# Performance work log

Measured on AMD Instinct MI355X. Metric: run time of the kernel, lower is better.

## Reference

```python
import jax, jax.numpy as jnp
import numpy as np

BATCH = 1024
DIM = 1024      # input_size == hidden_size (required by h0 = z.repeat(...))
BAR = 32
EPS = 1e-5


def setup_inputs() -> dict:
    key = jax.random.key(0)
    ks = jax.random.split(key, 13)
    s_in = 1.0 / np.sqrt(DIM)
    return {
        "z": jax.random.normal(ks[0], (BATCH, DIM), dtype=jnp.float32),
        "bn_gamma": jnp.ones((DIM,), jnp.float32),
        "bn_beta": jnp.zeros((DIM,), jnp.float32),
        # PyTorch LSTM params, gate order (i, f, g, o), shape (4H, in)
        "W_ih0": jax.random.uniform(ks[1], (4 * DIM, DIM), jnp.float32, -s_in, s_in),
        "W_hh0": jax.random.uniform(ks[2], (4 * DIM, DIM), jnp.float32, -s_in, s_in),
        "b_ih0": jax.random.uniform(ks[3], (4 * DIM,), jnp.float32, -s_in, s_in),
        "b_hh0": jax.random.uniform(ks[4], (4 * DIM,), jnp.float32, -s_in, s_in),
        "W_ih1": jax.random.uniform(ks[5], (4 * DIM, DIM), jnp.float32, -s_in, s_in),
        "W_hh1": jax.random.uniform(ks[6], (4 * DIM, DIM), jnp.float32, -s_in, s_in),
        "b_ih1": jax.random.uniform(ks[7], (4 * DIM,), jnp.float32, -s_in, s_in),
        "b_hh1": jax.random.uniform(ks[8], (4 * DIM,), jnp.float32, -s_in, s_in),
        "W_lin": jax.random.uniform(ks[9], (DIM, DIM), jnp.float32, -s_in, s_in),
        "b_lin": jax.random.uniform(ks[10], (DIM,), jnp.float32, -s_in, s_in),
    }


def _lstm_cell(x_proj, h, c, W_hh, b_hh):
    # x_proj already contains x @ W_ih^T + b_ih
    gates = x_proj + h @ W_hh.T + b_hh          # (B, 4H)
    i, f, g, o = jnp.split(gates, 4, axis=-1)   # PyTorch gate order i,f,g,o
    c_new = jax.nn.sigmoid(f) * c + jax.nn.sigmoid(i) * jnp.tanh(g)
    h_new = jax.nn.sigmoid(o) * jnp.tanh(c_new)
    return h_new, c_new


def reference(z, bn_gamma, bn_beta, W_ih0, W_hh0, b_ih0, b_hh0,
              W_ih1, W_hh1, b_ih1, b_hh1, W_lin, b_lin):
    # BatchNorm1d in training mode (batch statistics, biased variance)
    mean = jnp.mean(z, axis=0)
    var = jnp.var(z, axis=0)
    zn = (z - mean) * jax.lax.rsqrt(var + EPS) * bn_gamma + bn_beta  # (B, D)

    # h0 = c0 = zn for both layers (init_hidden repeats z num_hidden times)
    # Layer-0 input is the constant zn every step -> precompute its projection
    x0_proj = zn @ W_ih0.T + b_ih0  # (B, 4H)

    def step(carry, _):
        h0, c0, h1, c1 = carry
        h0, c0 = _lstm_cell(x0_proj, h0, c0, W_hh0, b_hh0)
        x1_proj = h0 @ W_ih1.T + b_ih1
        h1, c1 = _lstm_cell(x1_proj, h1, c1, W_hh1, b_hh1)
        return (h0, c0, h1, c1), h1

    _, feats = jax.lax.scan(step, (zn, zn, zn, zn), None, length=BAR)
    feat = jnp.transpose(feats, (1, 0, 2))      # (B, bar, H)
    return feat @ W_lin.T + b_lin
```

## Files before the change

kernel.cpp:

```cpp
#include <hip/hip_runtime.h>

#define DEV __device__ __forceinline__

typedef unsigned short u16;
using bf16x8 = __attribute__((ext_vector_type(8))) __bf16;
using f32x4  = __attribute__((ext_vector_type(4))) float;

DEV u16 f2bf(float f){
  unsigned u = __float_as_uint(f);
  u += 0x7fffu + ((u >> 16) & 1u);
  return (u16)(u >> 16);
}
DEV float sigf(float x){ return 1.f / (1.f + __expf(-x)); }
DEV float tanh_(float x){ return 2.f / (1.f + __expf(-2.f*x)) - 1.f; }

DEV void async16(const u16* g, u16* l){
  __builtin_amdgcn_global_load_lds(
      (const __attribute__((address_space(1))) unsigned int*)g,
      (__attribute__((address_space(3))) unsigned int*)l, 16, 0, 0);
}

__global__ void bn_stats(const float* __restrict__ z, float* __restrict__ ps, float* __restrict__ pq){
  int bx = blockIdx.x; int rg = bx >> 2, cg = bx & 3;
  int c = cg*256 + threadIdx.x;
  float s = 0.f, q = 0.f;
  for (int r = rg*64; r < rg*64 + 64; ++r){ float v = z[r*1024 + c]; s += v; q += v*v; }
  ps[rg*1024 + c] = s; pq[rg*1024 + c] = q;
}

__global__ void bn_fin(const float* __restrict__ ps, const float* __restrict__ pq,
                       const float* __restrict__ gam, const float* __restrict__ bet,
                       float* __restrict__ sc, float* __restrict__ sh){
  int c = blockIdx.x*256 + threadIdx.x;
  float s = 0.f, q = 0.f;
  for (int rg = 0; rg < 16; ++rg){ s += ps[rg*1024 + c]; q += pq[rg*1024 + c]; }
  float mean = s * (1.f/1024.f);
  float var  = q * (1.f/1024.f) - mean*mean;
  float k = gam[c] * rsqrtf(var + 1e-5f);
  sc[c] = k; sh[c] = bet[c] - mean*k;
}

__global__ void bn_norm(const float* __restrict__ z, const float* __restrict__ sc, const float* __restrict__ sh,
                        u16* __restrict__ h0, u16* __restrict__ h1,
                        float* __restrict__ c0, float* __restrict__ c1){
  int bx = blockIdx.x; int rg = bx >> 2, cg = bx & 3;
  int c = cg*256 + threadIdx.x;
  float k = sc[c], b = sh[c];
  for (int r = rg*64; r < rg*64 + 64; ++r){
    float v = z[r*1024 + c]*k + b;
    u16 hv = f2bf(v);
    h0[r*1024 + c] = hv; h1[r*1024 + c] = hv;
    c0[r*1024 + c] = v;  c1[r*1024 + c] = v;
  }
}

__global__ void pack_w(const float* __restrict__ src0, const float* __restrict__ src1,
                       int KloA, int K, int permute, u16* __restrict__ dst){
  int c = blockIdx.x*4 + (threadIdx.x >> 6);
  int lane = threadIdx.x & 63;
  int j = c & 3, wn = (c>>2)&1, ksub = (c>>3)&1;
  int rest = c >> 4;
  int nkt = K >> 6;
  int kt = rest % nkt, bx = rest / nkt;
  int rn = bx*128 + wn*64 + j*16 + (lane & 15);
  int row = rn;
  if (permute){ int gate=(rn>>4)&3; int u=(rn&15)|((rn>>6)<<4); row=(gate<<10)+u; }
  int k0 = kt*64 + ksub*32 + (lane>>4)*8;
  const float* s; int kk;
  if (k0 < KloA){ s = src0; kk = k0; } else { s = src1; kk = k0 - KloA; }
  const float4* v = (const float4*)(s + (size_t)row*1024 + kk);
  float4 a = v[0], b = v[1];
  ushort4 o0; o0.x=f2bf(a.x); o0.y=f2bf(a.y); o0.z=f2bf(a.z); o0.w=f2bf(a.w);
  ushort4 o1; o1.x=f2bf(b.x); o1.y=f2bf(b.y); o1.z=f2bf(b.z); o1.w=f2bf(b.w);
  ushort4* d = (ushort4*)(dst + ((size_t)c<<9) + lane*8);
  d[0]=o0; d[1]=o1;
}

__global__ void bias_k(const float* __restrict__ bi0, const float* __restrict__ bh0,
                       const float* __restrict__ bi1, const float* __restrict__ bh1,
                       float* __restrict__ bx0, float* __restrict__ b1){
  int c = blockIdx.x*256 + threadIdx.x;
  int gate = (c>>4)&3; int u = (c&15) | ((c>>6)<<4); int r = (gate<<10) + u;
  bx0[c] = bi0[r] + bh0[r];
  b1[c]  = bi1[r] + bh1[r];
}

template<int MODE>
DEV void gemm_core(int bx, int by,
                   const u16* __restrict__ A0, const u16* __restrict__ A1, int KloA,
                   const u16* __restrict__ Bp, int K,
                   const float* __restrict__ add, float* __restrict__ cst,
                   u16* __restrict__ hout, u16* __restrict__ hout2,
                   float* __restrict__ outf,
                   u16* sA)
{
  const int t = threadIdx.x;
  const int lane = t & 63;
  const int w = t >> 6, wm = w >> 1, wn = w & 1;
  const int m0 = by*128, n0 = bx*128;

  f32x4 acc[4][4];
#pragma unroll
  for (int i = 0; i < 4; ++i)
#pragma unroll
    for (int j = 0; j < 4; ++j) acc[i][j] = (f32x4){0.f,0.f,0.f,0.f};

  const int srow = t >> 3;
  const int kswz = (((t & 7) ^ ((t >> 3) & 7)) << 3);
  const int nkt = K >> 6;

  auto stageA = [&](int kt, int b){
    const int k0 = kt << 6;
    const u16* aPart; int kk;
    if (k0 < KloA){ aPart = A0; kk = k0; } else { aPart = A1; kk = k0 - KloA; }
    u16* dst = sA + b*8192;
#pragma unroll
    for (int p = 0; p < 4; ++p)
      async16(aPart + (size_t)(m0 + p*32 + srow)*1024 + kk + kswz,
              dst + p*2048 + t*8);
  };

  const u16* BpL = Bp + lane*8;
  auto loadB = [&](bf16x8* b, int kt, int ksub){
    const u16* p = BpL + (((((size_t)bx*nkt + kt)*2 + ksub)*2 + wn) << 11);
#pragma unroll
    for (int j = 0; j < 4; ++j) b[j] = *(const bf16x8*)(p + (size_t)j*512);
  };

  const int rsel = lane >> 4;
  const int rxor = lane & 7;

  bf16x8 bP[4], bQ[4];
  stageA(0, 0); stageA(1, 1);
  loadB(bP, 0, 0);
  asm volatile("s_waitcnt vmcnt(0)" ::: "memory");
  __builtin_amdgcn_sched_barrier(0);
  __builtin_amdgcn_s_barrier();
  __builtin_amdgcn_sched_barrier(0);

  for (int kt = 0; kt < nkt; ++kt){
    const u16* pA = sA + (kt % 3)*8192;
    loadB(bQ, kt, 1);
    {
      bf16x8 af[4];
#pragma unroll
      for (int i = 0; i < 4; ++i){
        int ra = wm*64 + i*16 + (lane & 15);
        int sl = ((0*4 + rsel) ^ rxor) << 3;
        af[i] = *(const bf16x8*)&pA[ra*64 + sl];
      }
      __builtin_amdgcn_s_setprio(1);
#pragma unroll
      for (int i = 0; i < 4; ++i)
#pragma unroll
        for (int j = 0; j < 4; ++j)
          acc[i][j] = __builtin_amdgcn_mfma_f32_16x16x32_bf16(af[i], bP[j], acc[i][j], 0, 0, 0);
      __builtin_amdgcn_s_setprio(0);
    }
    {
      int ktn = (kt + 1 < nkt) ? kt + 1 : nkt - 1;
      int kts = (kt + 2 < nkt) ? kt + 2 : nkt - 1;
      loadB(bP, ktn, 0);
      stageA(kts, (kt + 2) % 3);
      bf16x8 af[4];
#pragma unroll
      for (int i = 0; i < 4; ++i){
        int ra = wm*64 + i*16 + (lane & 15);
        int sl = ((1*4 + rsel) ^ rxor) << 3;
        af[i] = *(const bf16x8*)&pA[ra*64 + sl];
      }
      __builtin_amdgcn_s_setprio(1);
#pragma unroll
      for (int i = 0; i < 4; ++i)
#pragma unroll
        for (int j = 0; j < 4; ++j)
          acc[i][j] = __builtin_amdgcn_mfma_f32_16x16x32_bf16(af[i], bQ[j], acc[i][j], 0, 0, 0);
      __builtin_amdgcn_s_setprio(0);
    }
    asm volatile("s_waitcnt vmcnt(8)" ::: "memory");
    __builtin_amdgcn_sched_barrier(0);
    __builtin_amdgcn_s_barrier();
    __builtin_amdgcn_sched_barrier(0);
  }

  const int s  = lane & 15;
  const int rq = (lane >> 4) * 4;

  if constexpr (MODE == 0 || MODE == 3){
    const int ldc = (MODE == 0) ? 4096 : 1024;
#pragma unroll
    for (int j = 0; j < 4; ++j){
      int col = n0 + wn*64 + j*16 + s;
      float bj = add[col];
#pragma unroll
      for (int i = 0; i < 4; ++i){
        int rowb = m0 + wm*64 + i*16 + rq;
#pragma unroll
        for (int r = 0; r < 4; ++r)
          outf[(size_t)(rowb + r)*ldc + col] = acc[i][j][r] + bj;
      }
    }
  } else {
    const int u = s + ((bx*2 + wn) << 4);
    int cidx[4]; float bj[4];
#pragma unroll
    for (int j = 0; j < 4; ++j){
      cidx[j] = n0 + wn*64 + j*16 + s;
      if (MODE == 2) bj[j] = add[cidx[j]];
    }
#pragma unroll
    for (int i = 0; i < 4; ++i){
      int rowb = m0 + wm*64 + i*16 + rq;
#pragma unroll
      for (int r = 0; r < 4; ++r){
        int row = rowb + r;
        float g0, g1, g2, g3;
        if (MODE == 1){
          const float* xp = add + (size_t)row*4096;
          g0 = acc[i][0][r] + xp[cidx[0]];
          g1 = acc[i][1][r] + xp[cidx[1]];
          g2 = acc[i][2][r] + xp[cidx[2]];
          g3 = acc[i][3][r] + xp[cidx[3]];
        } else {
          g0 = acc[i][0][r] + bj[0];
          g1 = acc[i][1][r] + bj[1];
          g2 = acc[i][2][r] + bj[2];
          g3 = acc[i][3][r] + bj[3];
        }
        float ig = sigf(g0), fg = sigf(g1), gg = tanh_(g2), og = sigf(g3);
        size_t si = (size_t)row*1024 + u;
        float cn = fg * cst[si] + ig * gg;
        cst[si] = cn;
        float hn = og * tanh_(cn);
        u16 hb = f2bf(hn);
        hout[si] = hb;
        if (MODE == 2) hout2[(size_t)row*32768 + u] = hb;
      }
    }
  }
}

template<int MODE, int SWZ>
__global__ __launch_bounds__(256)
void gemm_k(const u16* __restrict__ A0, const u16* __restrict__ Bp, int K,
            const float* __restrict__ add, float* __restrict__ outf)
{
  __shared__ __align__(16) u16 sA[3*8192];
  int bx = blockIdx.x, by = blockIdx.y;
  if constexpr (SWZ){
    int lin = by * (int)gridDim.x + bx;
    int xcd = lin & 7, idx = lin >> 3;
    by = xcd*32 + (idx >> 3);
    bx = idx & 7;
  }
  gemm_core<MODE>(bx, by, A0, nullptr, 1<<20, Bp, K, add,
                  nullptr, nullptr, nullptr, outf, sA);
}

__global__ __launch_bounds__(256)
void fused_step(const u16* __restrict__ h0in, const u16* __restrict__ h1in,
                const u16* __restrict__ Whh0p, const u16* __restrict__ W1p,
                const float* __restrict__ X0p, const float* __restrict__ B1,
                float* __restrict__ C0, float* __restrict__ C1,
                u16* __restrict__ h0out, u16* __restrict__ h1out,
                u16* __restrict__ feats, int roles)
{
  __shared__ __align__(16) u16 sA[3*8192];
  int by = blockIdx.y, isL0;
  if (roles == 0){ isL0 = (by >= 8); by &= 7; }
  else isL0 = (roles == 1);
  if (isL0)
    gemm_core<1>(blockIdx.x, by, h0in, nullptr, 1<<20, Whh0p, 1024, X0p,
                 C0, h0out, nullptr, nullptr, sA);
  else
    gemm_core<2>(blockIdx.x, by, h0in, h1in, 1024, W1p, 2048, B1,
                 C1, h1out, feats, nullptr, sA);
}

extern "C" void kernel_launch(void* const* d_in, const int* in_sizes, int n_in,
                              void* d_out, int out_size, void* d_ws, size_t ws_size,
                              hipStream_t stream)
{
  (void)in_sizes; (void)n_in; (void)out_size; (void)ws_size;
  const float* z    = (const float*)d_in[0];
  const float* gam  = (const float*)d_in[1];
  const float* bet  = (const float*)d_in[2];
  const float* Wih0 = (const float*)d_in[3];
  const float* Whh0 = (const float*)d_in[4];
  const float* bih0 = (const float*)d_in[5];
  const float* bhh0 = (const float*)d_in[6];
  const float* Wih1 = (const float*)d_in[7];
  const float* Whh1 = (const float*)d_in[8];
  const float* bih1 = (const float*)d_in[9];
  const float* bhh1 = (const float*)d_in[10];
  const float* Wlin = (const float*)d_in[11];
  const float* blin = (const float*)d_in[12];
  float* out = (float*)d_out;

  char* p = (char*)d_ws;
  auto alloc = [&](size_t b) -> void* { void* r = (void*)p; p += (b + 255) & ~(size_t)255; return r; };
  u16*  Wih0p = (u16*)alloc((size_t)4096*1024*2);
  u16*  Whh0p = (u16*)alloc((size_t)4096*1024*2);
  u16*  W1p   = (u16*)alloc((size_t)4096*2048*2);
  u16*  Wlinp = (u16*)alloc((size_t)1024*1024*2);
  float* Bx0  = (float*)alloc(4096*4);
  float* B1   = (float*)alloc(4096*4);
  float* X0p  = (float*)alloc((size_t)1024*4096*4);
  u16*  H0a   = (u16*)alloc((size_t)1024*1024*2);
  u16*  H0b   = (u16*)alloc((size_t)1024*1024*2);
  u16*  H1a   = (u16*)alloc((size_t)1024*1024*2);
  u16*  H1b   = (u16*)alloc((size_t)1024*1024*2);
  float* C0   = (float*)alloc((size_t)1024*1024*4);
  float* C1   = (float*)alloc((size_t)1024*1024*4);
  u16*  Feats = (u16*)alloc((size_t)1024*32*1024*2);
  float* PS   = (float*)alloc(16*1024*4);
  float* PQ   = (float*)alloc(16*1024*4);
  float* Sc   = (float*)alloc(1024*4);
  float* Sh   = (float*)alloc(1024*4);

  bn_stats<<<64, 256, 0, stream>>>(z, PS, PQ);
  bn_fin<<<4, 256, 0, stream>>>(PS, PQ, gam, bet, Sc, Sh);
  bn_norm<<<64, 256, 0, stream>>>(z, Sc, Sh, H0a, H1a, C0, C1);
  pack_w<<<2048, 256, 0, stream>>>(Wih0, Wih0, 1<<20, 1024, 1, Wih0p);
  pack_w<<<2048, 256, 0, stream>>>(Whh0, Whh0, 1<<20, 1024, 1, Whh0p);
  pack_w<<<4096, 256, 0, stream>>>(Wih1, Whh1, 1024, 2048, 1, W1p);
  pack_w<<< 512, 256, 0, stream>>>(Wlin, Wlin, 1<<20, 1024, 0, Wlinp);
  bias_k<<<16, 256, 0, stream>>>(bih0, bhh0, bih1, bhh1, Bx0, B1);

  gemm_k<0,0><<<dim3(32,8), 256, 0, stream>>>(H0a, Wih0p, 1024, Bx0, X0p);

  u16* h0b[2] = {H0a, H0b};
  u16* h1b[2] = {H1a, H1b};

  fused_step<<<dim3(32,8), 256, 0, stream>>>(h0b[0], nullptr, Whh0p, W1p, X0p, B1,
                                             C0, C1, h0b[1], nullptr, nullptr, 1);
  for (int t = 0; t < 31; ++t){
    fused_step<<<dim3(32,16), 256, 0, stream>>>(
        h0b[(t+1)&1], h1b[t&1], Whh0p, W1p, X0p, B1,
        C0, C1, h0b[t&1], h1b[(t+1)&1], Feats + (size_t)t*1024, 0);
  }
  fused_step<<<dim3(32,8), 256, 0, stream>>>(h0b[0], h1b[1], Whh0p, W1p, X0p, B1,
                                             C0, C1, nullptr, h1b[0], Feats + (size_t)31*1024, 2);

  gemm_k<3,1><<<dim3(8,256), 256, 0, stream>>>(Feats, Wlinp, 1024, blin, out);
}
```

Measured before the change: 1.482 ms.

## Enlarge GEMM block tile to 256x128 with 8 waves and double-buffered LDS

Changes the GEMM tile from 128x128 with 4 waves to 256x128 with 8 waves. Each wave now owns 32 rows by all 128 columns, so every wave loads the full B slice, and the packed weight layout is changed to match. The A staging moves from a triple buffer to a double buffer, the grids are halved, and launch bounds are set to 512 threads with 2 blocks per SM. The intent is more A reuse per weight fetch and fewer blocks per step, at the cost of more registers per wave, a shallower prefetch pipeline and fewer blocks in flight (256 per fused step instead of 512).

```diff
diff --git a/kernel.cpp b/kernel.cpp
--- a/kernel.cpp
+++ b/kernel.cpp
@@ -58,17 +58,17 @@
                        int KloA, int K, int permute, u16* __restrict__ dst){
   int c = blockIdx.x*4 + (threadIdx.x >> 6);
   int lane = threadIdx.x & 63;
-  int j = c & 3, wn = (c>>2)&1, ksub = (c>>3)&1;
+  int j = c & 7, ksub = (c>>3)&1;
   int rest = c >> 4;
   int nkt = K >> 6;
   int kt = rest % nkt, bx = rest / nkt;
-  int rn = bx*128 + wn*64 + j*16 + (lane & 15);
+  int rn = bx*128 + j*16 + (lane & 15);
   int row = rn;
   if (permute){ int gate=(rn>>4)&3; int u=(rn&15)|((rn>>6)<<4); row=(gate<<10)+u; }
   int k0 = kt*64 + ksub*32 + (lane>>4)*8;
-  const float* s; int kk;
-  if (k0 < KloA){ s = src0; kk = k0; } else { s = src1; kk = k0 - KloA; }
-  const float4* v = (const float4*)(s + (size_t)row*1024 + kk);
+  const float* sp; int kk;
+  if (k0 < KloA){ sp = src0; kk = k0; } else { sp = src1; kk = k0 - KloA; }
+  const float4* v = (const float4*)(sp + (size_t)row*1024 + kk);
   float4 a = v[0], b = v[1];
   ushort4 o0; o0.x=f2bf(a.x); o0.y=f2bf(a.y); o0.z=f2bf(a.z); o0.w=f2bf(a.w);
   ushort4 o1; o1.x=f2bf(b.x); o1.y=f2bf(b.y); o1.z=f2bf(b.z); o1.w=f2bf(b.w);
@@ -96,16 +96,15 @@
 {
   const int t = threadIdx.x;
   const int lane = t & 63;
-  const int w = t >> 6, wm = w >> 1, wn = w & 1;
-  const int m0 = by*128, n0 = bx*128;
-
-  f32x4 acc[4][4];
-#pragma unroll
-  for (int i = 0; i < 4; ++i)
-#pragma unroll
-    for (int j = 0; j < 4; ++j) acc[i][j] = (f32x4){0.f,0.f,0.f,0.f};
-
-  const int srow = t >> 3;
+  const int wm = t >> 6;
+  const int m0 = by*256, n0 = bx*128;
+
+  f32x4 acc[2][8];
+#pragma unroll
+  for (int i = 0; i < 2; ++i)
+#pragma unroll
+    for (int j = 0; j < 8; ++j) acc[i][j] = (f32x4){0.f,0.f,0.f,0.f};
+
   const int kswz = (((t & 7) ^ ((t >> 3) & 7)) << 3);
   const int nkt = K >> 6;
 
@@ -113,25 +112,25 @@
     const int k0 = kt << 6;
     const u16* aPart; int kk;
     if (k0 < KloA){ aPart = A0; kk = k0; } else { aPart = A1; kk = k0 - KloA; }
-    u16* dst = sA + b*8192;
+    u16* dst = sA + b*16384;
 #pragma unroll
     for (int p = 0; p < 4; ++p)
-      async16(aPart + (size_t)(m0 + p*32 + srow)*1024 + kk + kswz,
-              dst + p*2048 + t*8);
+      async16(aPart + (size_t)(m0 + p*64 + (t>>3))*1024 + kk + kswz,
+              dst + p*4096 + t*8);
   };
 
   const u16* BpL = Bp + lane*8;
   auto loadB = [&](bf16x8* b, int kt, int ksub){
-    const u16* p = BpL + (((((size_t)bx*nkt + kt)*2 + ksub)*2 + wn) << 11);
-#pragma unroll
-    for (int j = 0; j < 4; ++j) b[j] = *(const bf16x8*)(p + (size_t)j*512);
+    const u16* p = BpL + ((((size_t)bx*nkt + kt)*2 + ksub) << 12);
+#pragma unroll
+    for (int j = 0; j < 8; ++j) b[j] = *(const bf16x8*)(p + (size_t)j*512);
   };
 
   const int rsel = lane >> 4;
   const int rxor = lane & 7;
 
-  bf16x8 bP[4], bQ[4];
-  stageA(0, 0); stageA(1, 1);
+  bf16x8 bP[8], bQ[8];
+  stageA(0, 0);
   loadB(bP, 0, 0);
   asm volatile("s_waitcnt vmcnt(0)" ::: "memory");
   __builtin_amdgcn_sched_barrier(0);
@@ -139,41 +138,41 @@
   __builtin_amdgcn_sched_barrier(0);
 
   for (int kt = 0; kt < nkt; ++kt){
-    const u16* pA = sA + (kt % 3)*8192;
+    const u16* pA = sA + (kt & 1)*16384;
     loadB(bQ, kt, 1);
+    { int kts = (kt + 1 < nkt) ? kt + 1 : nkt - 1;
+      stageA(kts, (kt + 1) & 1); }
     {
-      bf16x8 af[4];
-#pragma unroll
-      for (int i = 0; i < 4; ++i){
-        int ra = wm*64 + i*16 + (lane & 15);
+      bf16x8 af[2];
+#pragma unroll
+      for (int i = 0; i < 2; ++i){
+        int ra = wm*32 + i*16 + (lane & 15);
         int sl = ((0*4 + rsel) ^ rxor) << 3;
         af[i] = *(const bf16x8*)&pA[ra*64 + sl];
       }
       __builtin_amdgcn_s_setprio(1);
 #pragma unroll
-      for (int i = 0; i < 4; ++i)
-#pragma unroll
-        for (int j = 0; j < 4; ++j)
+      for (int i = 0; i < 2; ++i)
+#pragma unroll
+        for (int j = 0; j < 8; ++j)
           acc[i][j] = __builtin_amdgcn_mfma_f32_16x16x32_bf16(af[i], bP[j], acc[i][j], 0, 0, 0);
       __builtin_amdgcn_s_setprio(0);
     }
+    { int ktn = (kt + 1 < nkt) ? kt + 1 : nkt - 1;
+      loadB(bP, ktn, 0); }
     {
-      int ktn = (kt + 1 < nkt) ? kt + 1 : nkt - 1;
-      int kts = (kt + 2 < nkt) ? kt + 2 : nkt - 1;
-      loadB(bP, ktn, 0);
-      stageA(kts, (kt + 2) % 3);
-      bf16x8 af[4];
-#pragma unroll
-      for (int i = 0; i < 4; ++i){
-        int ra = wm*64 + i*16 + (lane & 15);
+      bf16x8 af[2];
+#pragma unroll
+      for (int i = 0; i < 2; ++i){
+        int ra = wm*32 + i*16 + (lane & 15);
         int sl = ((1*4 + rsel) ^ rxor) << 3;
         af[i] = *(const bf16x8*)&pA[ra*64 + sl];
       }
       __builtin_amdgcn_s_setprio(1);
 #pragma unroll
-      for (int i = 0; i < 4; ++i)
-#pragma unroll
-        for (int j = 0; j < 4; ++j)
+      for (int i = 0; i < 2; ++i)
+#pragma unroll
+        for (int j = 0; j < 8; ++j)
           acc[i][j] = __builtin_amdgcn_mfma_f32_16x16x32_bf16(af[i], bQ[j], acc[i][j], 0, 0, 0);
       __builtin_amdgcn_s_setprio(0);
     }
@@ -189,75 +188,78 @@
   if constexpr (MODE == 0 || MODE == 3){
     const int ldc = (MODE == 0) ? 4096 : 1024;
 #pragma unroll
-    for (int j = 0; j < 4; ++j){
-      int col = n0 + wn*64 + j*16 + s;
+    for (int j = 0; j < 8; ++j){
+      int col = n0 + j*16 + s;
       float bj = add[col];
 #pragma unroll
-      for (int i = 0; i < 4; ++i){
-        int rowb = m0 + wm*64 + i*16 + rq;
+      for (int i = 0; i < 2; ++i){
+        int rowb = m0 + wm*32 + i*16 + rq;
 #pragma unroll
         for (int r = 0; r < 4; ++r)
           outf[(size_t)(rowb + r)*ldc + col] = acc[i][j][r] + bj;
       }
     }
   } else {
-    const int u = s + ((bx*2 + wn) << 4);
-    int cidx[4]; float bj[4];
-#pragma unroll
-    for (int j = 0; j < 4; ++j){
-      cidx[j] = n0 + wn*64 + j*16 + s;
-      if (MODE == 2) bj[j] = add[cidx[j]];
-    }
-#pragma unroll
-    for (int i = 0; i < 4; ++i){
-      int rowb = m0 + wm*64 + i*16 + rq;
+    float bj[8];
+    if constexpr (MODE == 2){
+#pragma unroll
+      for (int j = 0; j < 8; ++j) bj[j] = add[n0 + j*16 + s];
+    }
+#pragma unroll
+    for (int i = 0; i < 2; ++i){
+      int rowb = m0 + wm*32 + i*16 + rq;
 #pragma unroll
       for (int r = 0; r < 4; ++r){
         int row = rowb + r;
-        float g0, g1, g2, g3;
-        if (MODE == 1){
-          const float* xp = add + (size_t)row*4096;
-          g0 = acc[i][0][r] + xp[cidx[0]];
-          g1 = acc[i][1][r] + xp[cidx[1]];
-          g2 = acc[i][2][r] + xp[cidx[2]];
-          g3 = acc[i][3][r] + xp[cidx[3]];
-        } else {
-          g0 = acc[i][0][r] + bj[0];
-          g1 = acc[i][1][r] + bj[1];
-          g2 = acc[i][2][r] + bj[2];
-          g3 = acc[i][3][r] + bj[3];
+#pragma unroll
+        for (int half = 0; half < 2; ++half){
+          float g0, g1, g2, g3;
+          if (MODE == 1){
+            const float* xp = add + (size_t)row*4096 + n0;
+            g0 = acc[i][half*4+0][r] + xp[(half*4+0)*16 + s];
+            g1 = acc[i][half*4+1][r] + xp[(half*4+1)*16 + s];
+            g2 = acc[i][half*4+2][r] + xp[(half*4+2)*16 + s];
+            g3 = acc[i][half*4+3][r] + xp[(half*4+3)*16 + s];
+          } else {
+            g0 = acc[i][half*4+0][r] + bj[half*4+0];
+            g1 = acc[i][half*4+1][r] + bj[half*4+1];
+            g2 = acc[i][half*4+2][r] + bj[half*4+2];
+            g3 = acc[i][half*4+3][r] + bj[half*4+3];
+          }
+          float ig = sigf(g0), fg = sigf(g1), gg = tanh_(g2), og = sigf(g3);
+          int u = s + ((bx*2 + half) << 4);
+          size_t si = (size_t)row*1024 + u;
+          float cn = fg * cst[si] + ig * gg;
+          cst[si] = cn;
+          float hn = og * tanh_(cn);
+          u16 hb = f2bf(hn);
+          hout[si] = hb;
+          if (MODE == 2) hout2[(size_t)row*32768 + u] = hb;
         }
-        float ig = sigf(g0), fg = sigf(g1), gg = tanh_(g2), og = sigf(g3);
-        size_t si = (size_t)row*1024 + u;
-        float cn = fg * cst[si] + ig * gg;
-        cst[si] = cn;
-        float hn = og * tanh_(cn);
-        u16 hb = f2bf(hn);
-        hout[si] = hb;
-        if (MODE == 2) hout2[(size_t)row*32768 + u] = hb;
       }
     }
   }
 }
 
 template<int MODE, int SWZ>
-__global__ __launch_bounds__(256)
+__global__ __launch_bounds__(512, 2)
 void gemm_k(const u16* __restrict__ A0, const u16* __restrict__ Bp, int K,
             const float* __restrict__ add, float* __restrict__ outf)
 {
-  __shared__ __align__(16) u16 sA[3*8192];
+  __shared__ __align__(16) u16 sA[2*16384];
   int bx = blockIdx.x, by = blockIdx.y;
   if constexpr (SWZ){
     int lin = by * (int)gridDim.x + bx;
     int xcd = lin & 7, idx = lin >> 3;
-    by = xcd*32 + (idx >> 3);
+    int ypt = (int)gridDim.y >> 3;
+    by = xcd*ypt + (idx >> 3);
     bx = idx & 7;
   }
   gemm_core<MODE>(bx, by, A0, nullptr, 1<<20, Bp, K, add,
                   nullptr, nullptr, nullptr, outf, sA);
 }
 
-__global__ __launch_bounds__(256)
+__global__ __launch_bounds__(512, 2)
 void fused_step(const u16* __restrict__ h0in, const u16* __restrict__ h1in,
                 const u16* __restrict__ Whh0p, const u16* __restrict__ W1p,
                 const float* __restrict__ X0p, const float* __restrict__ B1,
@@ -265,9 +267,9 @@
                 u16* __restrict__ h0out, u16* __restrict__ h1out,
                 u16* __restrict__ feats, int roles)
 {
-  __shared__ __align__(16) u16 sA[3*8192];
+  __shared__ __align__(16) u16 sA[2*16384];
   int by = blockIdx.y, isL0;
-  if (roles == 0){ isL0 = (by >= 8); by &= 7; }
+  if (roles == 0){ isL0 = (by >= 4); by &= 3; }
   else isL0 = (roles == 1);
   if (isL0)
     gemm_core<1>(blockIdx.x, by, h0in, nullptr, 1<<20, Whh0p, 1024, X0p,
@@ -327,20 +329,20 @@
   pack_w<<< 512, 256, 0, stream>>>(Wlin, Wlin, 1<<20, 1024, 0, Wlinp);
   bias_k<<<16, 256, 0, stream>>>(bih0, bhh0, bih1, bhh1, Bx0, B1);
 
-  gemm_k<0,0><<<dim3(32,8), 256, 0, stream>>>(H0a, Wih0p, 1024, Bx0, X0p);
+  gemm_k<0,0><<<dim3(32,4), 512, 0, stream>>>(H0a, Wih0p, 1024, Bx0, X0p);
 
   u16* h0b[2] = {H0a, H0b};
   u16* h1b[2] = {H1a, H1b};
 
-  fused_step<<<dim3(32,8), 256, 0, stream>>>(h0b[0], nullptr, Whh0p, W1p, X0p, B1,
+  fused_step<<<dim3(32,4), 512, 0, stream>>>(h0b[0], nullptr, Whh0p, W1p, X0p, B1,
                                              C0, C1, h0b[1], nullptr, nullptr, 1);
   for (int t = 0; t < 31; ++t){
-    fused_step<<<dim3(32,16), 256, 0, stream>>>(
+    fused_step<<<dim3(32,8), 512, 0, stream>>>(
         h0b[(t+1)&1], h1b[t&1], Whh0p, W1p, X0p, B1,
         C0, C1, h0b[t&1], h1b[(t+1)&1], Feats + (size_t)t*1024, 0);
   }
-  fused_step<<<dim3(32,8), 256, 0, stream>>>(h0b[0], h1b[1], Whh0p, W1p, X0p, B1,
+  fused_step<<<dim3(32,4), 512, 0, stream>>>(h0b[0], h1b[1], Whh0p, W1p, X0p, B1,
                                              C0, C1, nullptr, h1b[0], Feats + (size_t)31*1024, 2);
 
-  gemm_k<3,1><<<dim3(8,256), 256, 0, stream>>>(Feats, Wlinp, 1024, blin, out);
-}
+  gemm_k<3,1><<<dim3(8,128), 512, 0, stream>>>(Feats, Wlinp, 1024, blin, out);
+}
```

New measurement: 2.130 ms. +43.7%, slower.

## Pre-pack activations in MFMA fragment layout and load A directly to registers

Applied to the files above, without the earlier changes.

Hidden states and the feature buffer are now written in a fragment-packed layout that matches the MFMA operand order. This lets the GEMM core load A fragments straight from global memory into registers, like B, and drops the LDS triple-buffer staging, the swizzle and the per-iteration block barriers. The fused step kernel also interleaves layer-0 and layer-1 blocks across the grid. The intent is to remove LDS traffic and barrier stalls and to raise occupancy, at the cost of each wave re-reading A from global memory or L2 instead of sharing it through LDS.

```diff
diff --git a/kernel.cpp b/kernel.cpp
--- a/kernel.cpp
+++ b/kernel.cpp
@@ -14,10 +14,9 @@
 DEV float sigf(float x){ return 1.f / (1.f + __expf(-x)); }
 DEV float tanh_(float x){ return 2.f / (1.f + __expf(-2.f*x)) - 1.f; }
 
-DEV void async16(const u16* g, u16* l){
-  __builtin_amdgcn_global_load_lds(
-      (const __attribute__((address_space(1))) unsigned int*)g,
-      (__attribute__((address_space(3))) unsigned int*)l, 16, 0, 0);
+DEV void wpack(u16* __restrict__ b, int row, int u, u16 v){
+  size_t c = ((size_t)(row >> 4) * 32 + (u >> 5)) << 9;
+  b[c + (((row & 15) | (((u >> 3) & 3) << 4)) << 3) + (u & 7)] = v;
 }
 
 __global__ void bn_stats(const float* __restrict__ z, float* __restrict__ ps, float* __restrict__ pq){
@@ -49,7 +48,7 @@
   for (int r = rg*64; r < rg*64 + 64; ++r){
     float v = z[r*1024 + c]*k + b;
     u16 hv = f2bf(v);
-    h0[r*1024 + c] = hv; h1[r*1024 + c] = hv;
+    wpack(h0, r, c, hv); wpack(h1, r, c, hv);
     c0[r*1024 + c] = v;  c1[r*1024 + c] = v;
   }
 }
@@ -66,9 +65,9 @@
   int row = rn;
   if (permute){ int gate=(rn>>4)&3; int u=(rn&15)|((rn>>6)<<4); row=(gate<<10)+u; }
   int k0 = kt*64 + ksub*32 + (lane>>4)*8;
-  const float* s; int kk;
-  if (k0 < KloA){ s = src0; kk = k0; } else { s = src1; kk = k0 - KloA; }
-  const float4* v = (const float4*)(s + (size_t)row*1024 + kk);
+  const float* sp; int kk;
+  if (k0 < KloA){ sp = src0; kk = k0; } else { sp = src1; kk = k0 - KloA; }
+  const float4* v = (const float4*)(sp + (size_t)row*1024 + kk);
   float4 a = v[0], b = v[1];
   ushort4 o0; o0.x=f2bf(a.x); o0.y=f2bf(a.y); o0.z=f2bf(a.z); o0.w=f2bf(a.w);
   ushort4 o1; o1.x=f2bf(b.x); o1.y=f2bf(b.y); o1.z=f2bf(b.z); o1.w=f2bf(b.w);
@@ -90,9 +89,8 @@
                    const u16* __restrict__ A0, const u16* __restrict__ A1, int KloA,
                    const u16* __restrict__ Bp, int K,
                    const float* __restrict__ add, float* __restrict__ cst,
-                   u16* __restrict__ hout, u16* __restrict__ hout2,
-                   float* __restrict__ outf,
-                   u16* sA)
+                   u16* __restrict__ hout, u16* __restrict__ hout2, int tstep,
+                   float* __restrict__ outf)
 {
   const int t = threadIdx.x;
   const int lane = t & 63;
@@ -105,19 +103,16 @@
 #pragma unroll
     for (int j = 0; j < 4; ++j) acc[i][j] = (f32x4){0.f,0.f,0.f,0.f};
 
-  const int srow = t >> 3;
-  const int kswz = (((t & 7) ^ ((t >> 3) & 7)) << 3);
   const int nkt = K >> 6;
-
-  auto stageA = [&](int kt, int b){
+  const int rblk0 = (m0 >> 4) + wm*4;
+
+  auto loadA = [&](bf16x8* a, int kt, int ksub){
     const int k0 = kt << 6;
-    const u16* aPart; int kk;
-    if (k0 < KloA){ aPart = A0; kk = k0; } else { aPart = A1; kk = k0 - KloA; }
-    u16* dst = sA + b*8192;
-#pragma unroll
-    for (int p = 0; p < 4; ++p)
-      async16(aPart + (size_t)(m0 + p*32 + srow)*1024 + kk + kswz,
-              dst + p*2048 + t*8);
+    const u16* base; int ktl;
+    if (k0 < KloA){ base = A0; ktl = kt; } else { base = A1; ktl = kt - (KloA >> 6); }
+    const u16* p = base + (((size_t)rblk0*32 + ktl*2 + ksub) << 9) + lane*8;
+#pragma unroll
+    for (int i = 0; i < 4; ++i) a[i] = *(const bf16x8*)(p + (size_t)i*16384);
   };
 
   const u16* BpL = Bp + lane*8;
@@ -127,60 +122,27 @@
     for (int j = 0; j < 4; ++j) b[j] = *(const bf16x8*)(p + (size_t)j*512);
   };
 
-  const int rsel = lane >> 4;
-  const int rxor = lane & 7;
-
-  bf16x8 bP[4], bQ[4];
-  stageA(0, 0); stageA(1, 1);
-  loadB(bP, 0, 0);
-  asm volatile("s_waitcnt vmcnt(0)" ::: "memory");
-  __builtin_amdgcn_sched_barrier(0);
-  __builtin_amdgcn_s_barrier();
-  __builtin_amdgcn_sched_barrier(0);
+  bf16x8 aP[4], aQ[4], bP[4], bQ[4];
+  loadA(aP, 0, 0); loadB(bP, 0, 0);
 
   for (int kt = 0; kt < nkt; ++kt){
-    const u16* pA = sA + (kt % 3)*8192;
-    loadB(bQ, kt, 1);
-    {
-      bf16x8 af[4];
-#pragma unroll
-      for (int i = 0; i < 4; ++i){
-        int ra = wm*64 + i*16 + (lane & 15);
-        int sl = ((0*4 + rsel) ^ rxor) << 3;
-        af[i] = *(const bf16x8*)&pA[ra*64 + sl];
-      }
-      __builtin_amdgcn_s_setprio(1);
-#pragma unroll
-      for (int i = 0; i < 4; ++i)
-#pragma unroll
-        for (int j = 0; j < 4; ++j)
-          acc[i][j] = __builtin_amdgcn_mfma_f32_16x16x32_bf16(af[i], bP[j], acc[i][j], 0, 0, 0);
-      __builtin_amdgcn_s_setprio(0);
-    }
-    {
-      int ktn = (kt + 1 < nkt) ? kt + 1 : nkt - 1;
-      int kts = (kt + 2 < nkt) ? kt + 2 : nkt - 1;
-      loadB(bP, ktn, 0);
-      stageA(kts, (kt + 2) % 3);
-      bf16x8 af[4];
-#pragma unroll
-      for (int i = 0; i < 4; ++i){
-        int ra = wm*64 + i*16 + (lane & 15);
-        int sl = ((1*4 + rsel) ^ rxor) << 3;
-        af[i] = *(const bf16x8*)&pA[ra*64 + sl];
-      }
-      __builtin_amdgcn_s_setprio(1);
-#pragma unroll
-      for (int i = 0; i < 4; ++i)
-#pragma unroll
-        for (int j = 0; j < 4; ++j)
-          acc[i][j] = __builtin_amdgcn_mfma_f32_16x16x32_bf16(af[i], bQ[j], acc[i][j], 0, 0, 0);
-      __builtin_amdgcn_s_setprio(0);
-    }
-    asm volatile("s_waitcnt vmcnt(8)" ::: "memory");
-    __builtin_amdgcn_sched_barrier(0);
-    __builtin_amdgcn_s_barrier();
-    __builtin_amdgcn_sched_barrier(0);
+    loadA(aQ, kt, 1); loadB(bQ, kt, 1);
+    __builtin_amdgcn_s_setprio(1);
+#pragma unroll
+    for (int i = 0; i < 4; ++i)
+#pragma unroll
+      for (int j = 0; j < 4; ++j)
+        acc[i][j] = __builtin_amdgcn_mfma_f32_16x16x32_bf16(aP[i], bP[j], acc[i][j], 0, 0, 0);
+    __builtin_amdgcn_s_setprio(0);
+    { int ktn = (kt + 1 < nkt) ? kt + 1 : nkt - 1;
+      loadA(aP, ktn, 0); loadB(bP, ktn, 0); }
+    __builtin_amdgcn_s_setprio(1);
+#pragma unroll
+    for (int i = 0; i < 4; ++i)
+#pragma unroll
+      for (int j = 0; j < 4; ++j)
+        acc[i][j] = __builtin_amdgcn_mfma_f32_16x16x32_bf16(aQ[i], bQ[j], acc[i][j], 0, 0, 0);
+    __builtin_amdgcn_s_setprio(0);
   }
 
   const int s  = lane & 15;
@@ -233,8 +195,11 @@
         cst[si] = cn;
         float hn = og * tanh_(cn);
         u16 hb = f2bf(hn);
-        hout[si] = hb;
-        if (MODE == 2) hout2[(size_t)row*32768 + u] = hb;
+        wpack(hout, row, u, hb);
+        if (MODE == 2){
+          size_t cch = ((size_t)(row*2 + (tstep >> 4))*32 + (u >> 5)) << 9;
+          hout2[cch + (((tstep & 15) | (((u >> 3) & 3) << 4)) << 3) + (u & 7)] = hb;
+        }
       }
     }
   }
@@ -245,7 +210,6 @@
 void gemm_k(const u16* __restrict__ A0, const u16* __restrict__ Bp, int K,
             const float* __restrict__ add, float* __restrict__ outf)
 {
-  __shared__ __align__(16) u16 sA[3*8192];
   int bx = blockIdx.x, by = blockIdx.y;
   if constexpr (SWZ){
     int lin = by * (int)gridDim.x + bx;
@@ -254,7 +218,7 @@
     bx = idx & 7;
   }
   gemm_core<MODE>(bx, by, A0, nullptr, 1<<20, Bp, K, add,
-                  nullptr, nullptr, nullptr, outf, sA);
+                  nullptr, nullptr, nullptr, 0, outf);
 }
 
 __global__ __launch_bounds__(256)
@@ -263,18 +227,23 @@
                 const float* __restrict__ X0p, const float* __restrict__ B1,
                 float* __restrict__ C0, float* __restrict__ C1,
                 u16* __restrict__ h0out, u16* __restrict__ h1out,
-                u16* __restrict__ feats, int roles)
+                u16* __restrict__ feats, int tstep, int roles)
 {
-  __shared__ __align__(16) u16 sA[3*8192];
-  int by = blockIdx.y, isL0;
-  if (roles == 0){ isL0 = (by >= 8); by &= 7; }
-  else isL0 = (roles == 1);
+  int bx, by, isL0;
+  if (roles == 0){
+    int lin = blockIdx.y * (int)gridDim.x + blockIdx.x;
+    isL0 = lin & 1;
+    int tile = lin >> 1;
+    by = tile >> 5; bx = tile & 31;
+  } else {
+    isL0 = (roles == 1); by = blockIdx.y; bx = blockIdx.x;
+  }
   if (isL0)
-    gemm_core<1>(blockIdx.x, by, h0in, nullptr, 1<<20, Whh0p, 1024, X0p,
-                 C0, h0out, nullptr, nullptr, sA);
+    gemm_core<1>(bx, by, h0in, nullptr, 1<<20, Whh0p, 1024, X0p,
+                 C0, h0out, nullptr, 0, nullptr);
   else
-    gemm_core<2>(blockIdx.x, by, h0in, h1in, 1024, W1p, 2048, B1,
-                 C1, h1out, feats, nullptr, sA);
+    gemm_core<2>(bx, by, h0in, h1in, 1024, W1p, 2048, B1,
+                 C1, h1out, feats, tstep, nullptr);
 }
 
 extern "C" void kernel_launch(void* const* d_in, const int* in_sizes, int n_in,
@@ -333,14 +302,14 @@
   u16* h1b[2] = {H1a, H1b};
 
   fused_step<<<dim3(32,8), 256, 0, stream>>>(h0b[0], nullptr, Whh0p, W1p, X0p, B1,
-                                             C0, C1, h0b[1], nullptr, nullptr, 1);
+                                             C0, C1, h0b[1], nullptr, nullptr, 0, 1);
   for (int t = 0; t < 31; ++t){
     fused_step<<<dim3(32,16), 256, 0, stream>>>(
         h0b[(t+1)&1], h1b[t&1], Whh0p, W1p, X0p, B1,
-        C0, C1, h0b[t&1], h1b[(t+1)&1], Feats + (size_t)t*1024, 0);
+        C0, C1, h0b[t&1], h1b[(t+1)&1], Feats, t, 0);
   }
   fused_step<<<dim3(32,8), 256, 0, stream>>>(h0b[0], h1b[1], Whh0p, W1p, X0p, B1,
-                                             C0, C1, nullptr, h1b[0], Feats + (size_t)31*1024, 2);
+                                             C0, C1, nullptr, h1b[0], Feats, 31, 2);
 
   gemm_k<3,1><<<dim3(8,256), 256, 0, stream>>>(Feats, Wlinp, 1024, blin, out);
 }
```

New measurement: 1.703 ms. +14.9%, slower.
